# Kernel optimization log

Hardware: AMD Instinct MI355X
Metric: run time of the kernel (lower is better)

The kernel has to match this reference:

```python
import jax, jax.numpy as jnp
import numpy as np

VOCAB, H, HALF = 64, 64, 32
B, L = 256, 2048
LN_EPS = 1e-5


def _normalize(x):
    # F.normalize: x / max(||x||_2, 1e-12)
    n = jnp.linalg.norm(x, axis=-1, keepdims=True)
    return x / jnp.maximum(n, 1e-12)


def setup_inputs() -> dict:
    key = jax.random.key(0)
    ks = jax.random.split(key, 12)
    def lin(k, fin, fout):
        return jax.random.normal(k, (fin, fout), jnp.float32) / np.sqrt(fin)
    return {
        "seq": jax.random.randint(ks[0], (B, L), 0, VOCAB),
        "embed": jax.random.normal(ks[1], (VOCAB, H), jnp.float32) * 0.02,
        "w1": lin(ks[2], H, 2 * H), "b1": jnp.zeros((2 * H,), jnp.float32),
        "w2": lin(ks[3], 2 * H, H), "b2": jnp.zeros((H,), jnp.float32),
        "ln_g": jnp.ones((H,), jnp.float32), "ln_b": jnp.zeros((H,), jnp.float32),
        "ws": lin(ks[4], H, HALF), "bs": jnp.zeros((HALF,), jnp.float32),
        "we": lin(ks[5], H, HALF), "be": jnp.zeros((HALF,), jnp.float32),
        "wrp": lin(ks[6], 2 * HALF, H), "brp": jnp.zeros((H,), jnp.float32),
        "wout": lin(ks[7], H, VOCAB), "bout": jnp.zeros((VOCAB,), jnp.float32),
    }


def reference(seq, embed, w1, b1, w2, b2, ln_g, ln_b, ws, bs, we, be, wrp, brp, wout, bout):
    b, l = seq.shape
    h = embed[seq]  # [B,L,H]
    ff = jax.nn.relu(h @ w1 + b1) @ w2 + b2
    x = h + ff
    mu = jnp.mean(x, axis=-1, keepdims=True)
    var = jnp.mean((x - mu) ** 2, axis=-1, keepdims=True)
    h = (x - mu) * jax.lax.rsqrt(var + LN_EPS) * ln_g + ln_b  # [B,L,H]

    # precompute projections for the L-1 update steps
    hs = h[:, : l - 1] @ ws + bs           # [B,L-1,HALF]
    he = h[:, : l - 1] @ we + be
    k_s = _normalize(hs)
    k_e = _normalize(he)
    coef = (jnp.arange(1, l, dtype=h.dtype) / l)  # (t+1)/L

    def step(carry, inp):
        Ms, Me = carry
        ks_t, ke_t, hs_t, he_t, c = inp
        vps = jnp.einsum('bij,bj->bi', Ms, ks_t)
        vpe = jnp.einsum('bij,bj->bi', Me, ke_t)
        Ms = Ms + (hs_t - vps)[:, :, None] * ks_t[:, None, :]
        Me = Me + c * (he_t - vpe)[:, :, None] * ke_t[:, None, :]
        return (Ms, Me), None

    M0 = jnp.zeros((b, HALF, HALF), h.dtype)
    xs = (jnp.swapaxes(k_s, 0, 1), jnp.swapaxes(k_e, 0, 1),
          jnp.swapaxes(hs, 0, 1), jnp.swapaxes(he, 0, 1), coef)
    (Ms, Me), _ = jax.lax.scan(step, (M0, M0), xs)

    q = h[:, -1, :]
    qs = _normalize(q @ ws + bs)
    qe = _normalize(q @ we + be)
    rs = jnp.einsum('bij,bj->bi', Ms, qs)
    re = jnp.einsum('bij,bj->bi', Me, qe)
    r = jnp.concatenate([rs, re], axis=-1)  # [B,2*HALF]
    return (r @ wrp + brp) @ wout + bout     # [B,VOCAB]
```

## Files before the change

### kernel.cpp

```cpp
#include <hip/hip_runtime.h>
#include <hip/hip_bf16.h>


#define L_SEQ 2048
#define NPOS  2047

__device__ __forceinline__ float rdlane(float v, int l) {
    return __int_as_float(__builtin_amdgcn_readlane(__float_as_int(v), l));
}

__global__ void build_tables(const float* __restrict__ embed,
                             const float* __restrict__ w1, const float* __restrict__ b1,
                             const float* __restrict__ w2, const float* __restrict__ b2,
                             const float* __restrict__ ln_g, const float* __restrict__ ln_b,
                             const float* __restrict__ ws, const float* __restrict__ bs,
                             const float* __restrict__ we, const float* __restrict__ be,
                             float* __restrict__ tabs) {
    const int v = blockIdx.x;
    const int t = threadIdx.x;
    __shared__ float sh_h[64];
    __shared__ float sh_a[128];
    __shared__ float sh_x[64];

    sh_h[t] = embed[v * 64 + t];
    __syncthreads();

    float acc0 = b1[t], acc1 = b1[t + 64];
    #pragma unroll 8
    for (int k = 0; k < 64; ++k) {
        const float hv = sh_h[k];
        acc0 += hv * w1[k * 128 + t];
        acc1 += hv * w1[k * 128 + t + 64];
    }
    sh_a[t]      = fmaxf(acc0, 0.f);
    sh_a[t + 64] = fmaxf(acc1, 0.f);
    __syncthreads();

    float x = sh_h[t] + b2[t];
    #pragma unroll 8
    for (int k = 0; k < 128; ++k) x += sh_a[k] * w2[k * 64 + t];

    float mu = x;
    for (int m = 1; m <= 32; m <<= 1) mu += __shfl_xor(mu, m);
    mu *= (1.f / 64.f);
    const float dx = x - mu;
    float var = dx * dx;
    for (int m = 1; m <= 32; m <<= 1) var += __shfl_xor(var, m);
    var *= (1.f / 64.f);
    const float hln = dx * rsqrtf(var + 1e-5f) * ln_g[t] + ln_b[t];
    sh_x[t] = hln;
    __syncthreads();

    const int j   = t & 31;
    const int mem = t >> 5;
    const float* W  = mem ? we : ws;
    const float* Bv = mem ? be : bs;
    float p = Bv[j];
    #pragma unroll 8
    for (int k = 0; k < 64; ++k) p += sh_x[k] * W[k * 32 + j];

    float nn = p * p;
    for (int m = 1; m <= 16; m <<= 1) nn += __shfl_xor(nn, m);
    const float kn = p / fmaxf(sqrtf(nn), 1e-12f);

    tabs[(mem * 64 + v) * 32 + j]        = kn;
    tabs[4096 + (mem * 64 + v) * 32 + j] = p;
}

__global__ void gram_kernel(const float* __restrict__ tabs, float* __restrict__ gout) {
    const int v  = blockIdx.x;
    const int tt = threadIdx.x;
    const int m  = tt >> 6, w = tt & 63;
    __shared__ float kv[64];
    if (tt < 64) kv[tt] = tabs[((tt >> 5) * 64 + v) * 32 + (tt & 31)];
    __syncthreads();
    const float* kw  = &tabs[(m * 64 + w) * 32];
    const float* kvm = &kv[m * 32];
    float acc = 0.f;
    #pragma unroll 8
    for (int j = 0; j < 32; ++j) acc += kvm[j] * kw[j];
    gout[m * 4096 + v * 64 + w] = acc;
}

__global__ void __launch_bounds__(128, 1) scan_kernel(const int* __restrict__ seq,
                                                      const float* __restrict__ tabs,
                                                      float* __restrict__ rbuf) {
    const int b    = blockIdx.x;
    const int tid  = threadIdx.x;
    const int m    = tid >> 6;
    const int lane = tid & 63;
    const int q    = lane & 31;

    __shared__ float gt [2 * 64 * 65];
    __shared__ float hsh[2 * 64 * 32];

    for (int i = tid; i < 8192; i += 128) {
        const int mm = i >> 12, v = (i >> 6) & 63, ww = i & 63;
        gt[mm * 4160 + v * 65 + ww] = tabs[16384 + i];
    }
    for (int i = tid; i < 1024; i += 128)
        ((float4*)hsh)[i] = ((const float4*)(tabs + 4096))[i];
    __syncthreads();

    const int*  srow  = seq + b * L_SEQ;
    const int   rowV  = m * 4160 + lane * 65;
    const float invL  = 1.0f / (float)L_SEQ;
    const bool  mF    = (m != 0);
    const float invLe = mF ? invL : 0.0f;

    const int tokL = srow[NPOS];
    float gf = gt[rowV + tokL];
    float W  = 0.f;

    {
        int tk[31]; float cg[31];
        #pragma unroll
        for (int j = 0; j < 31; ++j) tk[j] = srow[2016 + j];
        #pragma unroll
        for (int j = 0; j < 31; ++j) cg[j] = gt[rowV + tk[j]];
        __builtin_amdgcn_sched_barrier(0);
        const float cb = mF ? (float)(2016 + 1) * invL : 1.0f;
        #pragma unroll
        for (int j = 30; j >= 0; --j) {
            const float d = rdlane(gf, tk[j]);
            const float c = cb + (float)j * invLe;
            const float e = c * d;
            gf = fmaf(-e, cg[j], gf);
            W += (lane == tk[j]) ? e : 0.f;
        }
    }

    for (int pb = 1984; pb >= 0; pb -= 32) {
        if (__all(fabsf(gf) < 1e-6f)) break;

        int tk[32]; float cg[32];
        #pragma unroll
        for (int j = 0; j < 32; ++j) tk[j] = srow[pb + j];
        #pragma unroll
        for (int j = 0; j < 32; ++j) cg[j] = gt[rowV + tk[j]];
        __builtin_amdgcn_sched_barrier(0);

        const float cb = mF ? (float)(pb + 1) * invL : 1.0f;
        #pragma unroll
        for (int j = 31; j >= 0; --j) {
            const float d = rdlane(gf, tk[j]);
            const float c = cb + (float)j * invLe;
            const float e = c * d;
            gf = fmaf(-e, cg[j], gf);
            W += (lane == tk[j]) ? e : 0.f;
        }
    }

    float r = 0.f;
    #pragma unroll 8
    for (int v = 0; v < 64; ++v) {
        const float wv = rdlane(W, v);
        r = fmaf(wv, hsh[(m * 64 + v) * 32 + q], r);
    }

    if (lane < 32)
        rbuf[b * 64 + m * 32 + q] = r;
}

__global__ void out_kernel(const float* __restrict__ rbuf,
                           const float* __restrict__ wrp, const float* __restrict__ brp,
                           const float* __restrict__ wout, const float* __restrict__ bout,
                           float* __restrict__ out) {
    const int b = blockIdx.x;
    const int t = threadIdx.x;
    __shared__ float rsh[64];
    __shared__ float ysh[64];

    rsh[t] = rbuf[b * 64 + t];
    __syncthreads();

    float y = brp[t];
    #pragma unroll 8
    for (int k = 0; k < 64; ++k) y += rsh[k] * wrp[k * 64 + t];
    ysh[t] = y;
    __syncthreads();

    float o = bout[t];
    #pragma unroll 8
    for (int k = 0; k < 64; ++k) o += ysh[k] * wout[k * 64 + t];
    out[b * 64 + t] = o;
}

extern "C" void kernel_launch(void* const* d_in, const int* in_sizes, int n_in,
                              void* d_out, int out_size, void* d_ws, size_t ws_size,
                              hipStream_t stream) {
    const int*   seq   = (const int*)  d_in[0];
    const float* embed = (const float*)d_in[1];
    const float* w1    = (const float*)d_in[2];
    const float* b1    = (const float*)d_in[3];
    const float* w2    = (const float*)d_in[4];
    const float* b2    = (const float*)d_in[5];
    const float* ln_g  = (const float*)d_in[6];
    const float* ln_b  = (const float*)d_in[7];
    const float* ws    = (const float*)d_in[8];
    const float* bs    = (const float*)d_in[9];
    const float* we    = (const float*)d_in[10];
    const float* be    = (const float*)d_in[11];
    const float* wrp   = (const float*)d_in[12];
    const float* brp   = (const float*)d_in[13];
    const float* wout  = (const float*)d_in[14];
    const float* bout  = (const float*)d_in[15];

    float* tabs = (float*)d_ws;
    float* gout = tabs + 16384;
    float* rbuf = tabs + 24576;

    build_tables<<<64, 64, 0, stream>>>(embed, w1, b1, w2, b2, ln_g, ln_b,
                                        ws, bs, we, be, tabs);
    gram_kernel<<<64, 128, 0, stream>>>(tabs, gout);
    scan_kernel<<<256, 128, 0, stream>>>(seq, tabs, rbuf);
    out_kernel<<<256, 64, 0, stream>>>(rbuf, wrp, brp, wout, bout, (float*)d_out);
}
```

Baseline: 73.42 us.

## Double-buffer token and gram loads ahead of the serial backward chain

Result: slower. 78.47 us (+6.9%).

```diff
diff --git a/kernel.cpp b/kernel.cpp
--- a/kernel.cpp
+++ b/kernel.cpp
@@ -82,6 +82,33 @@
     gout[m * 4096 + v * 64 + w] = acc;
 }
 
+#define BATCH(PB, TK, CGP, CB)                                                \
+  do {                                                                        \
+    const int pb_ = (PB);                                                     \
+    _Pragma("unroll")                                                         \
+    for (int j = 0; j < 32; ++j)                                              \
+      TK[j] = __builtin_amdgcn_readfirstlane(srow[pb_ + j]);                  \
+    CB = mF ? (float)(pb_ + 1) * invL : 1.0f;                                 \
+    _Pragma("unroll")                                                         \
+    for (int j = 0; j < 32; ++j) {                                            \
+      const float g_ = gt[rowV + TK[j]];                                      \
+      const float c_ = CB + (float)j * invLe;                                 \
+      CGP[j] = c_ * g_;                                                       \
+    }                                                                         \
+  } while (0)
+
+#define CHAIN(TK, CGP, CB)                                                    \
+  do {                                                                        \
+    _Pragma("unroll")                                                         \
+    for (int j = 31; j >= 0; --j) {                                           \
+      const float d_ = rdlane(gf, TK[j]);                                     \
+      gf = fmaf(-d_, CGP[j], gf);                                             \
+      const float c_ = CB + (float)j * invLe;                                 \
+      const float e_ = c_ * d_;                                               \
+      W += (lane == TK[j]) ? e_ : 0.f;                                        \
+    }                                                                         \
+  } while (0)
+
 __global__ void __launch_bounds__(128, 1) scan_kernel(const int* __restrict__ seq,
                                                       const float* __restrict__ tabs,
                                                       float* __restrict__ rbuf) {
@@ -108,47 +135,45 @@
     const bool  mF    = (m != 0);
     const float invLe = mF ? invL : 0.0f;
 
-    const int tokL = srow[NPOS];
+    const int tokL = __builtin_amdgcn_readfirstlane(srow[NPOS]);
     float gf = gt[rowV + tokL];
     float W  = 0.f;
 
+    int   tkA[32], tkB[32];
+    float cgpA[32], cgpB[32];
+    float cbA, cbB;
+
+    BATCH(2016, tkA, cgpA, cbA);
+    cgpA[31] = 0.f;
+
     {
-        int tk[31]; float cg[31];
-        #pragma unroll
-        for (int j = 0; j < 31; ++j) tk[j] = srow[2016 + j];
-        #pragma unroll
-        for (int j = 0; j < 31; ++j) cg[j] = gt[rowV + tk[j]];
-        __builtin_amdgcn_sched_barrier(0);
-        const float cb = mF ? (float)(2016 + 1) * invL : 1.0f;
+        __builtin_amdgcn_sched_barrier(0);
         #pragma unroll
         for (int j = 30; j >= 0; --j) {
-            const float d = rdlane(gf, tk[j]);
-            const float c = cb + (float)j * invLe;
-            const float e = c * d;
-            gf = fmaf(-e, cg[j], gf);
-            W += (lane == tk[j]) ? e : 0.f;
+            const float d_ = rdlane(gf, tkA[j]);
+            gf = fmaf(-d_, cgpA[j], gf);
+            const float c_ = cbA + (float)j * invLe;
+            const float e_ = c_ * d_;
+            W += (lane == tkA[j]) ? e_ : 0.f;
         }
     }
 
-    for (int pb = 1984; pb >= 0; pb -= 32) {
+    BATCH(1984, tkB, cgpB, cbB);
+    for (int i = 0; i < 31; ++i) {
         if (__all(fabsf(gf) < 1e-6f)) break;
-
-        int tk[32]; float cg[32];
-        #pragma unroll
-        for (int j = 0; j < 32; ++j) tk[j] = srow[pb + j];
-        #pragma unroll
-        for (int j = 0; j < 32; ++j) cg[j] = gt[rowV + tk[j]];
-        __builtin_amdgcn_sched_barrier(0);
-
-        const float cb = mF ? (float)(pb + 1) * invL : 1.0f;
-        #pragma unroll
-        for (int j = 31; j >= 0; --j) {
-            const float d = rdlane(gf, tk[j]);
-            const float c = cb + (float)j * invLe;
-            const float e = c * d;
-            gf = fmaf(-e, cg[j], gf);
-            W += (lane == tk[j]) ? e : 0.f;
-        }
+        const int pbA = 1952 - 64 * i;
+        BATCH(pbA, tkA, cgpA, cbA);
+        __builtin_amdgcn_sched_barrier(0);
+        CHAIN(tkB, cgpB, cbB);
+        const int pbB = pbA - 32;
+        const int pbBc = (pbB >= 0) ? pbB : 0;
+        BATCH(pbBc, tkB, cgpB, cbB);
+        __builtin_amdgcn_sched_barrier(0);
+        CHAIN(tkA, cgpA, cbA);
+    }
+    if (!__all(fabsf(gf) < 1e-6f)) {
+        __builtin_amdgcn_sched_barrier(0);
+        CHAIN(tkB, cgpB, cbB);
     }
 
     float r = 0.f;
```

## Double-buffer token/gram loads in scan and fold output projection into chain

Applied to the files above, without the earlier changes.

Measured after the change: 93.36 us. 27.2% more time.

```diff
diff --git a/kernel.cpp b/kernel.cpp
--- a/kernel.cpp
+++ b/kernel.cpp
@@ -82,6 +82,48 @@
     gout[m * 4096 + v * 64 + w] = acc;
 }
 
+#define LOADTOKS(KK, TV) do {                                                 \
+    const uint4* p_ = (const uint4*)&seq16[(KK) << 4];                        \
+    TV[0] = p_[0]; TV[1] = p_[1]; TV[2] = p_[2]; TV[3] = p_[3]; } while (0)
+
+#define CONVERT(TV, TS) do {                                                  \
+    _Pragma("unroll")                                                         \
+    for (int i2 = 0; i2 < 4; ++i2) {                                          \
+      const unsigned wx_ = (unsigned)__builtin_amdgcn_readfirstlane((int)TV[i2].x); \
+      const unsigned wy_ = (unsigned)__builtin_amdgcn_readfirstlane((int)TV[i2].y); \
+      const unsigned wz_ = (unsigned)__builtin_amdgcn_readfirstlane((int)TV[i2].z); \
+      const unsigned ww_ = (unsigned)__builtin_amdgcn_readfirstlane((int)TV[i2].w); \
+      TS[8*i2+0] = (int)(wx_ & 0xffffu); TS[8*i2+1] = (int)(wx_ >> 16);       \
+      TS[8*i2+2] = (int)(wy_ & 0xffffu); TS[8*i2+3] = (int)(wy_ >> 16);       \
+      TS[8*i2+4] = (int)(wz_ & 0xffffu); TS[8*i2+5] = (int)(wz_ >> 16);       \
+      TS[8*i2+6] = (int)(ww_ & 0xffffu); TS[8*i2+7] = (int)(ww_ >> 16);       \
+    } } while (0)
+
+#define LOADRAW(TS, CG, HC) do {                                              \
+    _Pragma("unroll")                                                         \
+    for (int j = 0; j < 32; ++j) {                                            \
+      CG[j] = gt [rowV + TS[j]];                                              \
+      HC[j] = hsh[rowH + (TS[j] << 5)];                                       \
+    } } while (0)
+
+#define TOUCH(CG, HC) asm volatile("" :: "v"(CG[31]), "v"(HC[31]))
+
+#define PRESCALE(KB, CG, HC) do {                                             \
+    if (mF) { const float cb_ = (float)(32 * (KB) + 1) * invL;                \
+      _Pragma("unroll")                                                       \
+      for (int j = 0; j < 32; ++j) {                                          \
+        const float c_ = cb_ + (float)j * invL;                               \
+        CG[j] *= c_; HC[j] *= c_;                                             \
+      } } } while (0)
+
+#define CHAIN(TS, CG, HC, JTOP) do {                                          \
+    _Pragma("unroll")                                                         \
+    for (int j = (JTOP); j >= 0; --j) {                                       \
+      const float d_ = rdlane(gf, TS[j]);                                     \
+      gf = fmaf(-d_, CG[j], gf);                                              \
+      r  = fmaf( d_, HC[j], r);                                               \
+    } } while (0)
+
 __global__ void __launch_bounds__(128, 1) scan_kernel(const int* __restrict__ seq,
                                                       const float* __restrict__ tabs,
                                                       float* __restrict__ rbuf) {
@@ -91,8 +133,9 @@
     const int lane = tid & 63;
     const int q    = lane & 31;
 
-    __shared__ float gt [2 * 64 * 65];
-    __shared__ float hsh[2 * 64 * 32];
+    __shared__ float    gt  [2 * 64 * 65];
+    __shared__ float    hsh [2 * 64 * 32];
+    __shared__ unsigned seq16[1024];
 
     for (int i = tid; i < 8192; i += 128) {
         const int mm = i >> 12, v = (i >> 6) & 63, ww = i & 63;
@@ -100,62 +143,70 @@
     }
     for (int i = tid; i < 1024; i += 128)
         ((float4*)hsh)[i] = ((const float4*)(tabs + 4096))[i];
-    __syncthreads();
-
-    const int*  srow  = seq + b * L_SEQ;
-    const int   rowV  = m * 4160 + lane * 65;
-    const float invL  = 1.0f / (float)L_SEQ;
-    const bool  mF    = (m != 0);
-    const float invLe = mF ? invL : 0.0f;
-
-    const int tokL = srow[NPOS];
+    {
+        const int4* s4 = (const int4*)(seq + b * L_SEQ);
+        for (int i = tid; i < 512; i += 128) {
+            const int4 vv = s4[i];
+            seq16[2*i]     = (unsigned)vv.x | ((unsigned)vv.y << 16);
+            seq16[2*i + 1] = (unsigned)vv.z | ((unsigned)vv.w << 16);
+        }
+    }
+    __syncthreads();
+
+    const int   rowV = m * 4160 + lane * 65;
+    const int   rowH = m * 2048 + q;
+    const float invL = 1.0f / (float)L_SEQ;
+    const bool  mF   = (m != 0);
+
+    const int tokL = (int)((unsigned)__builtin_amdgcn_readfirstlane(
+                              (int)seq16[1023]) >> 16);
     float gf = gt[rowV + tokL];
-    float W  = 0.f;
-
-    {
-        int tk[31]; float cg[31];
-        #pragma unroll
-        for (int j = 0; j < 31; ++j) tk[j] = srow[2016 + j];
-        #pragma unroll
-        for (int j = 0; j < 31; ++j) cg[j] = gt[rowV + tk[j]];
+    float r  = 0.f;
+
+    uint4 tvE[4], tvO[4];
+    int   tsE[32], tsO[32];
+    float cgE[32], hcE[32], cgO[32], hcO[32];
+
+    LOADTOKS(63, tvO);
+    LOADTOKS(62, tvE);
+    CONVERT(tvO, tsO);
+    LOADRAW(tsO, cgO, hcO);
+    TOUCH(cgO, hcO);
+    PRESCALE(63, cgO, hcO);
+    CONVERT(tvE, tsE);
+    LOADTOKS(61, tvO);
+    LOADRAW(tsE, cgE, hcE);
+    __builtin_amdgcn_sched_barrier(0);
+    CHAIN(tsO, cgO, hcO, 30);
+
+    TOUCH(cgE, hcE);
+    PRESCALE(62, cgE, hcE);
+    CONVERT(tvO, tsO);
+    LOADTOKS(60, tvE);
+    LOADRAW(tsO, cgO, hcO);
+    __builtin_amdgcn_sched_barrier(0);
+    CHAIN(tsE, cgE, hcE, 31);
+
+    for (int k2 = 61; k2 >= 1; k2 -= 2) {
+        if (__all(fabsf(gf) < 1e-6f)) break;
+
+        TOUCH(cgO, hcO);
+        PRESCALE(k2, cgO, hcO);
+        CONVERT(tvE, tsE);
+        { const int kk = (k2 >= 2) ? k2 - 2 : 0; LOADTOKS(kk, tvO); }
+        LOADRAW(tsE, cgE, hcE);
         __builtin_amdgcn_sched_barrier(0);
-        const float cb = mF ? (float)(2016 + 1) * invL : 1.0f;
-        #pragma unroll
-        for (int j = 30; j >= 0; --j) {
-            const float d = rdlane(gf, tk[j]);
-            const float c = cb + (float)j * invLe;
-            const float e = c * d;
-            gf = fmaf(-e, cg[j], gf);
-            W += (lane == tk[j]) ? e : 0.f;
+        CHAIN(tsO, cgO, hcO, 31);
+
+        TOUCH(cgE, hcE);
+        PRESCALE(k2 - 1, cgE, hcE);
+        if (k2 > 1) {
+            CONVERT(tvO, tsO);
+            { const int kk = (k2 >= 3) ? k2 - 3 : 0; LOADTOKS(kk, tvE); }
+            LOADRAW(tsO, cgO, hcO);
         }
-    }
-
-    for (int pb = 1984; pb >= 0; pb -= 32) {
-        if (__all(fabsf(gf) < 1e-6f)) break;
-
-        int tk[32]; float cg[32];
-        #pragma unroll
-        for (int j = 0; j < 32; ++j) tk[j] = srow[pb + j];
-        #pragma unroll
-        for (int j = 0; j < 32; ++j) cg[j] = gt[rowV + tk[j]];
         __builtin_amdgcn_sched_barrier(0);
-
-        const float cb = mF ? (float)(pb + 1) * invL : 1.0f;
-        #pragma unroll
-        for (int j = 31; j >= 0; --j) {
-            const float d = rdlane(gf, tk[j]);
-            const float c = cb + (float)j * invLe;
-            const float e = c * d;
-            gf = fmaf(-e, cg[j], gf);
-            W += (lane == tk[j]) ? e : 0.f;
-        }
-    }
-
-    float r = 0.f;
-    #pragma unroll 8
-    for (int v = 0; v < 64; ++v) {
-        const float wv = rdlane(W, v);
-        r = fmaf(wv, hsh[(m * 64 + v) * 32 + q], r);
+        CHAIN(tsE, cgE, hcE, 31);
     }
 
     if (lane < 32)
```

## Block the backward Gram recurrence four steps at a time and accumulate output directly

Applied to the files above, without the earlier changes.

After: 92.41 us. 25.9% more time.

```diff
diff --git a/kernel.cpp b/kernel.cpp
--- a/kernel.cpp
+++ b/kernel.cpp
@@ -91,8 +91,9 @@
     const int lane = tid & 63;
     const int q    = lane & 31;
 
-    __shared__ float gt [2 * 64 * 65];
-    __shared__ float hsh[2 * 64 * 32];
+    __shared__ float    gt  [2 * 64 * 65];
+    __shared__ float    hsh [2 * 64 * 32];
+    __shared__ unsigned seq16[1024];
 
     for (int i = tid; i < 8192; i += 128) {
         const int mm = i >> 12, v = (i >> 6) & 63, ww = i & 63;
@@ -100,62 +101,97 @@
     }
     for (int i = tid; i < 1024; i += 128)
         ((float4*)hsh)[i] = ((const float4*)(tabs + 4096))[i];
-    __syncthreads();
-
-    const int*  srow  = seq + b * L_SEQ;
-    const int   rowV  = m * 4160 + lane * 65;
-    const float invL  = 1.0f / (float)L_SEQ;
-    const bool  mF    = (m != 0);
-    const float invLe = mF ? invL : 0.0f;
-
-    const int tokL = srow[NPOS];
+    {
+        const int4* s4 = (const int4*)(seq + b * L_SEQ);
+        for (int i = tid; i < 512; i += 128) {
+            const int4 vv = s4[i];
+            seq16[2*i]     = (unsigned)vv.x | ((unsigned)vv.y << 16);
+            seq16[2*i + 1] = (unsigned)vv.z | ((unsigned)vv.w << 16);
+        }
+    }
+    __syncthreads();
+
+    const int   rowV = m * 4160 + lane * 65;
+    const int   rowH = m * 2048 + q;
+    const float invL = 1.0f / (float)L_SEQ;
+    const bool  mF   = (m != 0);
+    const float step = mF ? invL : 0.0f;
+
+    const int tokL = (int)((unsigned)__builtin_amdgcn_readfirstlane(
+                              (int)seq16[1023]) >> 16);
     float gf = gt[rowV + tokL];
-    float W  = 0.f;
-
-    {
-        int tk[31]; float cg[31];
-        #pragma unroll
-        for (int j = 0; j < 31; ++j) tk[j] = srow[2016 + j];
-        #pragma unroll
-        for (int j = 0; j < 31; ++j) cg[j] = gt[rowV + tk[j]];
+    float r  = 0.f;
+
+    for (int pb = 2016; pb >= 0; pb -= 32) {
+        if (__all(fabsf(gf) < 1e-6f)) break;
+
+        int ts[32];
+        #pragma unroll
+        for (int w = 0; w < 16; ++w) {
+            const unsigned pw = (unsigned)__builtin_amdgcn_readfirstlane(
+                                    (int)seq16[(pb >> 1) + w]);
+            ts[2*w]     = (int)(pw & 0xffffu);
+            ts[2*w + 1] = (int)(pw >> 16);
+        }
+        float cgb[32], hcb[32];
+        #pragma unroll
+        for (int i = 0; i < 32; ++i) {
+            cgb[i] = gt [rowV + ts[i]];
+            hcb[i] = hsh[rowH + (ts[i] << 5)];
+        }
+        float G32[8], G31[8], G30[8], G21[8], G20[8], G10[8];
+        #pragma unroll
+        for (int k = 0; k < 8; ++k) {
+            const int i0 = 4*k, i1 = i0+1, i2 = i0+2, i3 = i0+3;
+            G32[k] = rdlane(cgb[i3], ts[i2]);
+            G31[k] = rdlane(cgb[i3], ts[i1]);
+            G30[k] = rdlane(cgb[i3], ts[i0]);
+            G21[k] = rdlane(cgb[i2], ts[i1]);
+            G20[k] = rdlane(cgb[i2], ts[i0]);
+            G10[k] = rdlane(cgb[i1], ts[i0]);
+        }
+        const float ctop = mF ? (float)(pb + 32) * invL : 1.0f;
+        const bool  topBlk = (pb == 2016);
+
         __builtin_amdgcn_sched_barrier(0);
-        const float cb = mF ? (float)(2016 + 1) * invL : 1.0f;
-        #pragma unroll
-        for (int j = 30; j >= 0; --j) {
-            const float d = rdlane(gf, tk[j]);
-            const float c = cb + (float)j * invLe;
-            const float e = c * d;
-            gf = fmaf(-e, cg[j], gf);
-            W += (lane == tk[j]) ? e : 0.f;
-        }
-    }
-
-    for (int pb = 1984; pb >= 0; pb -= 32) {
-        if (__all(fabsf(gf) < 1e-6f)) break;
-
-        int tk[32]; float cg[32];
-        #pragma unroll
-        for (int j = 0; j < 32; ++j) tk[j] = srow[pb + j];
-        #pragma unroll
-        for (int j = 0; j < 32; ++j) cg[j] = gt[rowV + tk[j]];
-        __builtin_amdgcn_sched_barrier(0);
-
-        const float cb = mF ? (float)(pb + 1) * invL : 1.0f;
-        #pragma unroll
-        for (int j = 31; j >= 0; --j) {
-            const float d = rdlane(gf, tk[j]);
-            const float c = cb + (float)j * invLe;
-            const float e = c * d;
-            gf = fmaf(-e, cg[j], gf);
-            W += (lane == tk[j]) ? e : 0.f;
-        }
-    }
-
-    float r = 0.f;
-    #pragma unroll 8
-    for (int v = 0; v < 64; ++v) {
-        const float wv = rdlane(W, v);
-        r = fmaf(wv, hsh[(m * 64 + v) * 32 + q], r);
+
+        float cRun = ctop;
+        #pragma unroll
+        for (int k = 7; k >= 0; --k) {
+            const int i0 = 4*k, i1 = i0+1, i2 = i0+2, i3 = i0+3;
+            float c3 = cRun;
+            if (k == 7) c3 = topBlk ? 0.f : c3;
+            const float c2 = cRun - step;
+            const float c1 = c2 - step;
+            const float c0 = c1 - step;
+            cRun = c0 - step;
+
+            const float a3 = rdlane(gf, ts[i3]);
+            const float a2 = rdlane(gf, ts[i2]);
+            const float a1 = rdlane(gf, ts[i1]);
+            const float a0 = rdlane(gf, ts[i0]);
+
+            const float e3 = c3 * a3;
+            const float d2 = a2 - G32[k] * e3;
+            const float e2 = c2 * d2;
+            const float t1 = fmaf(G21[k], e2, G31[k] * e3);
+            const float d1 = a1 - t1;
+            const float e1 = c1 * d1;
+            const float t0 = fmaf(G10[k], e1,
+                             fmaf(G20[k], e2, G30[k] * e3));
+            const float d0 = a0 - t0;
+            const float e0 = c0 * d0;
+
+            gf = fmaf(-e3, cgb[i3], gf);
+            gf = fmaf(-e2, cgb[i2], gf);
+            gf = fmaf(-e1, cgb[i1], gf);
+            gf = fmaf(-e0, cgb[i0], gf);
+
+            r  = fmaf(e3, hcb[i3], r);
+            r  = fmaf(e2, hcb[i2], r);
+            r  = fmaf(e1, hcb[i1], r);
+            r  = fmaf(e0, hcb[i0], r);
+        }
     }
 
     if (lane < 32)
```
